# Kernel optimization log

Measured on AMD Instinct MI355X. Metric: run time of the kernel, lower is better.

Reference implementation:

```python
import math
import jax, jax.numpy as jnp
import numpy as np

B, S, HID, NH = 4, 1024, 768, 12
D = HID // NH
R_ACT = 0.5
R_ATTN = 0.5


def act_prune_mask(a, ratio):
    # per-sample kth-smallest magnitude threshold (torch.kthvalue on flatten(1))
    n = int(np.prod(a.shape[1:]))
    k = int(np.clip(n * ratio, 1, n))
    mag = jnp.abs(a)
    thr = jnp.sort(mag.reshape(a.shape[0], -1), axis=1)[:, k - 1]
    thr = thr.reshape((a.shape[0],) + (1,) * (a.ndim - 1))
    return mag >= thr


def setup_inputs() -> dict:
    key = jax.random.key(0)
    ks = jax.random.split(key, 5)
    inp = {
        "hidden_states": jax.random.normal(ks[0], (B, S, HID), dtype=jnp.float32),
        "Wq": jax.random.normal(ks[1], (HID, HID), dtype=jnp.float32) * 0.02,
        "bq": jnp.zeros((HID,), dtype=jnp.float32),
        "Wk": jax.random.normal(ks[2], (HID, HID), dtype=jnp.float32) * 0.02,
        "bk": jnp.zeros((HID,), dtype=jnp.float32),
        "Wv": jax.random.normal(ks[3], (HID, HID), dtype=jnp.float32) * 0.02,
        "bv": jnp.zeros((HID,), dtype=jnp.float32),
        "Wo": jax.random.normal(ks[4], (HID, HID), dtype=jnp.float32) * 0.02,
        "bo": jnp.zeros((HID,), dtype=jnp.float32),
    }
    return inp


def reference(hidden_states, Wq, bq, Wk, bk, Wv, bv, Wo, bo):
    b, s, hid = hidden_states.shape

    # prune mask on input activations (saved for backward in the original; forward math unchanged)
    mask_h = act_prune_mask(hidden_states, R_ACT)
    _hs_prune = jnp.where(mask_h, hidden_states, 0.0)

    q = jnp.matmul(hidden_states, Wq.T) + bq
    k = jnp.matmul(hidden_states, Wk.T) + bk
    v = jnp.matmul(hidden_states, Wv.T) + bv

    def split_heads(x):
        return x.reshape(b, s, NH, D).transpose(0, 2, 1, 3)  # [B,H,S,D]

    q4, k4, v4 = split_heads(q), split_heads(k), split_heads(v)

    mask_q = act_prune_mask(q4, R_ACT)
    mask_k = act_prune_mask(k4, R_ACT)
    _qp = jnp.where(mask_q, q4, 0.0)
    _kp = jnp.where(mask_k, k4, 0.0)

    scores = jnp.einsum("bhqd,bhkd->bhqk", q4, k4) / math.sqrt(D)
    probs = jax.nn.softmax(scores, axis=-1)

    mask_p = act_prune_mask(probs, R_ATTN)
    _pp = jnp.where(mask_p, probs, 0.0)
    mask_v = act_prune_mask(v4, R_ACT)
    _vp = jnp.where(mask_v, v4, 0.0)

    ctx = jnp.einsum("bhqk,bhkd->bhqd", probs, v4)
    ctx = ctx.transpose(0, 2, 1, 3).reshape(b, s, hid)

    mask_c = act_prune_mask(ctx, R_ACT)
    _cp = jnp.where(mask_c, ctx, 0.0)

    out = jnp.matmul(ctx, Wo.T) + bo  # proj_dropout rate = 0.0 (identity)
    return (out, probs)  # vis=True -> weights = attention_probs
```

## Files before the change

kernel.cpp:

```cpp
#include <hip/hip_runtime.h>
#include <hip/hip_bf16.h>

typedef __attribute__((ext_vector_type(4))) float f32x4;
typedef __attribute__((ext_vector_type(8))) short bf16x8;
typedef __attribute__((ext_vector_type(4))) int i32x4;

#define SEQ 1024
#define HIDV 768
#define NH 12
#define HD 64
#define QBLK 64

static __device__ __forceinline__ unsigned short f2b(float f) {
  unsigned u = __builtin_bit_cast(unsigned, f);
  u = (u + 0x7fffu + ((u >> 16) & 1u)) >> 16;
  return (unsigned short)u;
}

static __device__ __forceinline__ void gl16(const unsigned short* g, unsigned short* l) {
  __builtin_amdgcn_global_load_lds(
      (const __attribute__((address_space(1))) unsigned int*)g,
      (__attribute__((address_space(3))) unsigned int*)l, 16, 0, 0);
}

static __device__ __forceinline__ void bar_lgkm() {
  asm volatile("s_waitcnt lgkmcnt(0)" ::: "memory");
  __builtin_amdgcn_sched_barrier(0);
  __builtin_amdgcn_s_barrier();
  __builtin_amdgcn_sched_barrier(0);
}
static __device__ __forceinline__ void bar_only() {
  __builtin_amdgcn_sched_barrier(0);
  __builtin_amdgcn_s_barrier();
  __builtin_amdgcn_sched_barrier(0);
}

__global__ __launch_bounds__(256) void convert_all(
    const float* __restrict__ X, const float* __restrict__ Wq,
    const float* __restrict__ Wk, const float* __restrict__ Wv,
    const float* __restrict__ Wo, unsigned short* __restrict__ dst) {
  long i = (long)blockIdx.x * 256 + threadIdx.x;
  const long N4 = (3145728L + 4 * 589824L) / 4;
  if (i >= N4) return;
  long e = i * 4;
  const float* src; long off;
  if (e < 3145728L)      { src = X;  off = e; }
  else if (e < 3735552L) { src = Wq; off = e - 3145728L; }
  else if (e < 4325376L) { src = Wk; off = e - 3735552L; }
  else if (e < 4915200L) { src = Wv; off = e - 4325376L; }
  else                   { src = Wo; off = e - 4915200L; }
  const float4 v = *reinterpret_cast<const float4*>(src + off);
  ushort4 o;
  o.x = f2b(v.x); o.y = f2b(v.y); o.z = f2b(v.z); o.w = f2b(v.w);
  *reinterpret_cast<ushort4*>(dst + e) = o;
}

__global__ __launch_bounds__(256) void qkv_gemm(
    const unsigned short* __restrict__ Xb,
    const unsigned short* __restrict__ Wqb, const unsigned short* __restrict__ Wkb,
    const unsigned short* __restrict__ Wvb,
    const float* __restrict__ bq, const float* __restrict__ bk, const float* __restrict__ bv,
    unsigned short* __restrict__ Qh, unsigned short* __restrict__ Kh,
    unsigned short* __restrict__ VT) {
  __shared__ __align__(16) unsigned short la[128 * 32];
  __shared__ __align__(16) unsigned short lb[128 * 32];
  const int z = blockIdx.z;
  const unsigned short* Wb = (z == 0) ? Wqb : (z == 1) ? Wkb : Wvb;
  const float* bias = (z == 0) ? bq : (z == 1) ? bk : bv;
  const int m0 = blockIdx.x * 128, n0 = blockIdx.y * 128;
  const int tid = threadIdx.x;
  const int wave = tid >> 6, lane = tid & 63, g = lane >> 4, c = lane & 15;
  const int wr = (wave >> 1) * 64, wc = (wave & 1) * 64;

  const int sr = wave * 16 + (lane >> 2);
  const int scol = (lane & 3) * 8;
  const unsigned short* Ag = &Xb[(size_t)(m0 + sr) * HIDV + scol];
  const unsigned short* Bg = &Wb[(size_t)(n0 + sr) * HIDV + scol];
  unsigned short* lA0 = &la[(wave * 16) * 32];
  unsigned short* lA1 = &la[(64 + wave * 16) * 32];
  unsigned short* lB0 = &lb[(wave * 16) * 32];
  unsigned short* lB1 = &lb[(64 + wave * 16) * 32];

  f32x4 acc[4][4] = {};
  for (int kt = 0; kt < HIDV; kt += 32) {
    __syncthreads();
    gl16(Ag + kt, lA0);
    gl16(Ag + (size_t)64 * HIDV + kt, lA1);
    gl16(Bg + kt, lB0);
    gl16(Bg + (size_t)64 * HIDV + kt, lB1);
    __syncthreads();
    bf16x8 af[4], bfr[4];
#pragma unroll
    for (int m = 0; m < 4; m++)
      af[m] = *reinterpret_cast<bf16x8*>(&la[(wr + m * 16 + c) * 32 + g * 8]);
#pragma unroll
    for (int n = 0; n < 4; n++)
      bfr[n] = *reinterpret_cast<bf16x8*>(&lb[(wc + n * 16 + c) * 32 + g * 8]);
#pragma unroll
    for (int m = 0; m < 4; m++)
#pragma unroll
      for (int n = 0; n < 4; n++)
        acc[m][n] = __builtin_amdgcn_mfma_f32_16x16x32_bf16(af[m], bfr[n], acc[m][n], 0, 0, 0);
  }
  float bv4[4];
#pragma unroll
  for (int n = 0; n < 4; n++) bv4[n] = bias[n0 + wc + n * 16 + c];
  if (z < 2) {
    unsigned short* dst = (z == 0) ? Qh : Kh;
#pragma unroll
    for (int m = 0; m < 4; m++) {
      int rb_ = m0 + wr + m * 16 + g * 4;
#pragma unroll
      for (int n = 0; n < 4; n++) {
        int col = n0 + wc + n * 16 + c;
        int h = col >> 6, d = col & 63;
#pragma unroll
        for (int r = 0; r < 4; r++) {
          int row = rb_ + r;
          int b = row >> 10, s = row & 1023;
          dst[((size_t)(b * NH + h) * SEQ + s) * HD + d] = f2b(acc[m][n][r] + bv4[n]);
        }
      }
    }
  } else {
#pragma unroll
    for (int m = 0; m < 4; m++) {
      int rb_ = m0 + wr + m * 16 + g * 4;
      int b = rb_ >> 10, s = rb_ & 1023;
#pragma unroll
      for (int n = 0; n < 4; n++) {
        int col = n0 + wc + n * 16 + c;
        int h = col >> 6, d = col & 63;
        ushort4 o;
        o.x = f2b(acc[m][n][0] + bv4[n]);
        o.y = f2b(acc[m][n][1] + bv4[n]);
        o.z = f2b(acc[m][n][2] + bv4[n]);
        o.w = f2b(acc[m][n][3] + bv4[n]);
        *reinterpret_cast<ushort4*>(&VT[((size_t)(b * NH + h) * HD + d) * SEQ + s]) = o;
      }
    }
  }
}

#define EXPC 0.18033688f
__global__ __launch_bounds__(256) void attn_fused(
    const unsigned short* __restrict__ Qh, const unsigned short* __restrict__ Kh,
    const unsigned short* __restrict__ VT,
    float* __restrict__ probs, unsigned short* __restrict__ CTX) {
  __shared__ __align__(16) unsigned short ldsk[2][64 * 72];
  __shared__ __align__(16) unsigned short ldsv[2][64 * 72];
  __shared__ __align__(16) unsigned short lp[64 * 72];
  const int bh = blockIdx.y, rb = blockIdx.x * QBLK;
  const int b = bh / NH, h = bh - b * NH;
  const unsigned short* Qp = Qh + (size_t)bh * SEQ * HD;
  const unsigned short* Kp = Kh + (size_t)bh * SEQ * HD;
  const unsigned short* Vp = VT + (size_t)bh * HD * SEQ;
  float* P = probs + (size_t)bh * SEQ * SEQ;
  const int tid = threadIdx.x, wave = tid >> 6, lane = tid & 63, g = lane >> 4, c = lane & 15;
  const int wrow = wave * 16;
  const int str = tid >> 3;
  const int stc = (tid & 7) * 8;

  bf16x8 aq[2];
#pragma unroll
  for (int ks = 0; ks < 2; ks++)
    aq[ks] = *reinterpret_cast<const bf16x8*>(&Qp[(size_t)(rb + wrow + c) * HD + ks * 32 + g * 8]);

  i32x4 kr0, kr1, vr0, vr1;
  kr0 = *reinterpret_cast<const i32x4*>(&Kp[(size_t)str * HD + stc]);
  kr1 = *reinterpret_cast<const i32x4*>(&Kp[(size_t)(str + 32) * HD + stc]);
  *reinterpret_cast<i32x4*>(&ldsk[0][str * 72 + stc]) = kr0;
  *reinterpret_cast<i32x4*>(&ldsk[0][(str + 32) * 72 + stc]) = kr1;
  bar_lgkm();

  float lsum = 0.f;
  for (int ct = 0; ct < 16; ct++) {
    const int cur = ct & 1;
    if (ct < 15) {
      kr0 = *reinterpret_cast<const i32x4*>(&Kp[(size_t)((ct + 1) * 64 + str) * HD + stc]);
      kr1 = *reinterpret_cast<const i32x4*>(&Kp[(size_t)((ct + 1) * 64 + str + 32) * HD + stc]);
    }
    f32x4 sreg[4] = {};
#pragma unroll
    for (int ks = 0; ks < 2; ks++) {
      bf16x8 kf[4];
#pragma unroll
      for (int kb = 0; kb < 4; kb++)
        kf[kb] = *reinterpret_cast<bf16x8*>(&ldsk[cur][(kb * 16 + c) * 72 + ks * 32 + g * 8]);
#pragma unroll
      for (int kb = 0; kb < 4; kb++)
        sreg[kb] = __builtin_amdgcn_mfma_f32_16x16x32_bf16(kf[kb], aq[ks], sreg[kb], 0, 0, 0);
    }
#pragma unroll
    for (int kb = 0; kb < 4; kb++)
#pragma unroll
      for (int r = 0; r < 4; r++)
        lsum += __builtin_amdgcn_exp2f(sreg[kb][r] * EXPC);
    if (ct < 15) {
      *reinterpret_cast<i32x4*>(&ldsk[cur ^ 1][str * 72 + stc]) = kr0;
      *reinterpret_cast<i32x4*>(&ldsk[cur ^ 1][(str + 32) * 72 + stc]) = kr1;
      bar_lgkm();
    }
  }
  float s = lsum;
  s += __shfl_xor(s, 16);
  s += __shfl_xor(s, 32);
  const float linv = 1.f / s;

  kr0 = *reinterpret_cast<const i32x4*>(&Kp[(size_t)str * HD + stc]);
  kr1 = *reinterpret_cast<const i32x4*>(&Kp[(size_t)(str + 32) * HD + stc]);
  vr0 = *reinterpret_cast<const i32x4*>(&Vp[(size_t)str * SEQ + stc]);
  vr1 = *reinterpret_cast<const i32x4*>(&Vp[(size_t)(str + 32) * SEQ + stc]);
  *reinterpret_cast<i32x4*>(&ldsk[0][str * 72 + stc]) = kr0;
  *reinterpret_cast<i32x4*>(&ldsk[0][(str + 32) * 72 + stc]) = kr1;
  *reinterpret_cast<i32x4*>(&ldsv[0][str * 72 + stc]) = vr0;
  *reinterpret_cast<i32x4*>(&ldsv[0][(str + 32) * 72 + stc]) = vr1;
  bar_lgkm();

  f32x4 acc[4] = {};
  for (int ct = 0; ct < 16; ct++) {
    const int cur = ct & 1;
    if (ct < 15) {
      kr0 = *reinterpret_cast<const i32x4*>(&Kp[(size_t)((ct + 1) * 64 + str) * HD + stc]);
      kr1 = *reinterpret_cast<const i32x4*>(&Kp[(size_t)((ct + 1) * 64 + str + 32) * HD + stc]);
      vr0 = *reinterpret_cast<const i32x4*>(&Vp[(size_t)str * SEQ + (ct + 1) * 64 + stc]);
      vr1 = *reinterpret_cast<const i32x4*>(&Vp[(size_t)(str + 32) * SEQ + (ct + 1) * 64 + stc]);
    }
    f32x4 sreg[4] = {};
#pragma unroll
    for (int ks = 0; ks < 2; ks++) {
      bf16x8 kf[4];
#pragma unroll
      for (int kb = 0; kb < 4; kb++)
        kf[kb] = *reinterpret_cast<bf16x8*>(&ldsk[cur][(kb * 16 + c) * 72 + ks * 32 + g * 8]);
#pragma unroll
      for (int kb = 0; kb < 4; kb++)
        sreg[kb] = __builtin_amdgcn_mfma_f32_16x16x32_bf16(kf[kb], aq[ks], sreg[kb], 0, 0, 0);
    }
    {
      float* Prow = &P[(size_t)(rb + wrow + c) * SEQ + ct * 64];
#pragma unroll
      for (int kb = 0; kb < 4; kb++) {
        f32x4 p;
#pragma unroll
        for (int r = 0; r < 4; r++)
          p[r] = __builtin_amdgcn_exp2f(sreg[kb][r] * EXPC) * linv;
        *reinterpret_cast<f32x4*>(&Prow[kb * 16 + g * 4]) = p;
        uint2 pk;
        pk.x = (unsigned)f2b(p[0]) | ((unsigned)f2b(p[1]) << 16);
        pk.y = (unsigned)f2b(p[2]) | ((unsigned)f2b(p[3]) << 16);
        *reinterpret_cast<uint2*>(&lp[(wrow + c) * 72 + kb * 16 + g * 4]) = pk;
      }
    }
    if (ct < 15) {
      *reinterpret_cast<i32x4*>(&ldsk[cur ^ 1][str * 72 + stc]) = kr0;
      *reinterpret_cast<i32x4*>(&ldsk[cur ^ 1][(str + 32) * 72 + stc]) = kr1;
      *reinterpret_cast<i32x4*>(&ldsv[cur ^ 1][str * 72 + stc]) = vr0;
      *reinterpret_cast<i32x4*>(&ldsv[cur ^ 1][(str + 32) * 72 + stc]) = vr1;
    }
    bar_lgkm();
#pragma unroll
    for (int ks = 0; ks < 2; ks++) {
      bf16x8 pa, vf[4];
      pa = *reinterpret_cast<bf16x8*>(&lp[(wrow + c) * 72 + ks * 32 + g * 8]);
#pragma unroll
      for (int db = 0; db < 4; db++)
        vf[db] = *reinterpret_cast<bf16x8*>(&ldsv[cur][(db * 16 + c) * 72 + ks * 32 + g * 8]);
#pragma unroll
      for (int db = 0; db < 4; db++)
        acc[db] = __builtin_amdgcn_mfma_f32_16x16x32_bf16(pa, vf[db], acc[db], 0, 0, 0);
    }
    bar_only();
  }

#pragma unroll
  for (int db = 0; db < 4; db++)
#pragma unroll
    for (int r = 0; r < 4; r++)
      lp[(wrow + g * 4 + r) * 72 + db * 16 + c] = f2b(acc[db][r]);
  bar_lgkm();
  {
    const int q = tid >> 2, seg = (tid & 3) * 16;
    const unsigned short* src = &lp[q * 72 + seg];
    unsigned short* dst = &CTX[(size_t)(b * SEQ + rb + q) * HIDV + h * HD + seg];
    i32x4 t0 = *reinterpret_cast<const i32x4*>(&src[0]);
    i32x4 t1 = *reinterpret_cast<const i32x4*>(&src[8]);
    *reinterpret_cast<i32x4*>(&dst[0]) = t0;
    *reinterpret_cast<i32x4*>(&dst[8]) = t1;
  }
}

__global__ __launch_bounds__(256) void proj_gemm(
    const unsigned short* __restrict__ Ab, const unsigned short* __restrict__ Wb,
    const float* __restrict__ bias, float* __restrict__ out) {
  __shared__ __align__(16) unsigned short la[128 * 32];
  __shared__ __align__(16) unsigned short lb[128 * 32];
  const int m0 = blockIdx.x * 128, n0 = blockIdx.y * 128;
  const int tid = threadIdx.x;
  const int wave = tid >> 6, lane = tid & 63, g = lane >> 4, c = lane & 15;
  const int wr = (wave >> 1) * 64, wc = (wave & 1) * 64;
  const int sr = wave * 16 + (lane >> 2);
  const int scol = (lane & 3) * 8;
  const unsigned short* Ag = &Ab[(size_t)(m0 + sr) * HIDV + scol];
  const unsigned short* Bg = &Wb[(size_t)(n0 + sr) * HIDV + scol];
  unsigned short* lA0 = &la[(wave * 16) * 32];
  unsigned short* lA1 = &la[(64 + wave * 16) * 32];
  unsigned short* lB0 = &lb[(wave * 16) * 32];
  unsigned short* lB1 = &lb[(64 + wave * 16) * 32];

  f32x4 acc[4][4] = {};
  for (int kt = 0; kt < HIDV; kt += 32) {
    __syncthreads();
    gl16(Ag + kt, lA0);
    gl16(Ag + (size_t)64 * HIDV + kt, lA1);
    gl16(Bg + kt, lB0);
    gl16(Bg + (size_t)64 * HIDV + kt, lB1);
    __syncthreads();
    bf16x8 af[4], bfr[4];
#pragma unroll
    for (int m = 0; m < 4; m++)
      af[m] = *reinterpret_cast<bf16x8*>(&la[(wr + m * 16 + c) * 32 + g * 8]);
#pragma unroll
    for (int n = 0; n < 4; n++)
      bfr[n] = *reinterpret_cast<bf16x8*>(&lb[(wc + n * 16 + c) * 32 + g * 8]);
#pragma unroll
    for (int m = 0; m < 4; m++)
#pragma unroll
      for (int n = 0; n < 4; n++)
        acc[m][n] = __builtin_amdgcn_mfma_f32_16x16x32_bf16(af[m], bfr[n], acc[m][n], 0, 0, 0);
  }
  float bv4[4];
#pragma unroll
  for (int n = 0; n < 4; n++) bv4[n] = bias[n0 + wc + n * 16 + c];
#pragma unroll
  for (int m = 0; m < 4; m++) {
    int rb_ = m0 + wr + m * 16 + g * 4;
#pragma unroll
    for (int n = 0; n < 4; n++) {
      int col = n0 + wc + n * 16 + c;
#pragma unroll
      for (int r = 0; r < 4; r++)
        out[(size_t)(rb_ + r) * HIDV + col] = acc[m][n][r] + bv4[n];
    }
  }
}

extern "C" void kernel_launch(void* const* d_in, const int* in_sizes, int n_in,
                              void* d_out, int out_size, void* d_ws, size_t ws_size,
                              hipStream_t stream) {
  const float* X  = (const float*)d_in[0];
  const float* Wq = (const float*)d_in[1];
  const float* bq = (const float*)d_in[2];
  const float* Wk = (const float*)d_in[3];
  const float* bk = (const float*)d_in[4];
  const float* Wv = (const float*)d_in[5];
  const float* bv = (const float*)d_in[6];
  const float* Wo = (const float*)d_in[7];
  const float* bo = (const float*)d_in[8];
  float* out = (float*)d_out;
  float* probs = out + 3145728;

  unsigned short* Xb  = (unsigned short*)d_ws;
  unsigned short* Wqb = Xb + 3145728;
  unsigned short* Wkb = Wqb + 589824;
  unsigned short* Wvb = Wkb + 589824;
  unsigned short* Wob = Wvb + 589824;
  unsigned short* Qh  = Wob + 589824;
  unsigned short* Kh  = Qh + 3145728;
  unsigned short* VT  = Kh + 3145728;
  unsigned short* CTX = VT + 3145728;

  convert_all<<<5376, 256, 0, stream>>>(X, Wq, Wk, Wv, Wo, Xb);
  qkv_gemm<<<dim3(32, 6, 3), 256, 0, stream>>>(Xb, Wqb, Wkb, Wvb, bq, bk, bv, Qh, Kh, VT);
  attn_fused<<<dim3(16, 48), 256, 0, stream>>>(Qh, Kh, VT, probs, CTX);
  proj_gemm<<<dim3(32, 6), 256, 0, stream>>>(CTX, Wob, bo, out);
}
```

Before: 126.9 us.

## Double-buffer GEMM LDS tiles and read attention K/V directly from global

```diff
diff --git a/kernel.cpp b/kernel.cpp
--- a/kernel.cpp
+++ b/kernel.cpp
@@ -21,18 +21,6 @@
   __builtin_amdgcn_global_load_lds(
       (const __attribute__((address_space(1))) unsigned int*)g,
       (__attribute__((address_space(3))) unsigned int*)l, 16, 0, 0);
-}
-
-static __device__ __forceinline__ void bar_lgkm() {
-  asm volatile("s_waitcnt lgkmcnt(0)" ::: "memory");
-  __builtin_amdgcn_sched_barrier(0);
-  __builtin_amdgcn_s_barrier();
-  __builtin_amdgcn_sched_barrier(0);
-}
-static __device__ __forceinline__ void bar_only() {
-  __builtin_amdgcn_sched_barrier(0);
-  __builtin_amdgcn_s_barrier();
-  __builtin_amdgcn_sched_barrier(0);
 }
 
 __global__ __launch_bounds__(256) void convert_all(
@@ -62,8 +50,8 @@
     const float* __restrict__ bq, const float* __restrict__ bk, const float* __restrict__ bv,
     unsigned short* __restrict__ Qh, unsigned short* __restrict__ Kh,
     unsigned short* __restrict__ VT) {
-  __shared__ __align__(16) unsigned short la[128 * 32];
-  __shared__ __align__(16) unsigned short lb[128 * 32];
+  __shared__ __align__(16) unsigned short la[2][128 * 32];
+  __shared__ __align__(16) unsigned short lb[2][128 * 32];
   const int z = blockIdx.z;
   const unsigned short* Wb = (z == 0) ? Wqb : (z == 1) ? Wkb : Wvb;
   const float* bias = (z == 0) ? bq : (z == 1) ? bk : bv;
@@ -76,31 +64,36 @@
   const int scol = (lane & 3) * 8;
   const unsigned short* Ag = &Xb[(size_t)(m0 + sr) * HIDV + scol];
   const unsigned short* Bg = &Wb[(size_t)(n0 + sr) * HIDV + scol];
-  unsigned short* lA0 = &la[(wave * 16) * 32];
-  unsigned short* lA1 = &la[(64 + wave * 16) * 32];
-  unsigned short* lB0 = &lb[(wave * 16) * 32];
-  unsigned short* lB1 = &lb[(64 + wave * 16) * 32];
+
+  gl16(Ag, &la[0][(wave * 16) * 32]);
+  gl16(Ag + (size_t)64 * HIDV, &la[0][(64 + wave * 16) * 32]);
+  gl16(Bg, &lb[0][(wave * 16) * 32]);
+  gl16(Bg + (size_t)64 * HIDV, &lb[0][(64 + wave * 16) * 32]);
+  __syncthreads();
 
   f32x4 acc[4][4] = {};
-  for (int kt = 0; kt < HIDV; kt += 32) {
-    __syncthreads();
-    gl16(Ag + kt, lA0);
-    gl16(Ag + (size_t)64 * HIDV + kt, lA1);
-    gl16(Bg + kt, lB0);
-    gl16(Bg + (size_t)64 * HIDV + kt, lB1);
-    __syncthreads();
+  for (int t = 0; t < 24; t++) {
+    const int cur = t & 1;
+    if (t < 23) {
+      const int kt = (t + 1) * 32;
+      gl16(Ag + kt, &la[cur ^ 1][(wave * 16) * 32]);
+      gl16(Ag + (size_t)64 * HIDV + kt, &la[cur ^ 1][(64 + wave * 16) * 32]);
+      gl16(Bg + kt, &lb[cur ^ 1][(wave * 16) * 32]);
+      gl16(Bg + (size_t)64 * HIDV + kt, &lb[cur ^ 1][(64 + wave * 16) * 32]);
+    }
     bf16x8 af[4], bfr[4];
 #pragma unroll
     for (int m = 0; m < 4; m++)
-      af[m] = *reinterpret_cast<bf16x8*>(&la[(wr + m * 16 + c) * 32 + g * 8]);
+      af[m] = *reinterpret_cast<bf16x8*>(&la[cur][(wr + m * 16 + c) * 32 + g * 8]);
 #pragma unroll
     for (int n = 0; n < 4; n++)
-      bfr[n] = *reinterpret_cast<bf16x8*>(&lb[(wc + n * 16 + c) * 32 + g * 8]);
+      bfr[n] = *reinterpret_cast<bf16x8*>(&lb[cur][(wc + n * 16 + c) * 32 + g * 8]);
 #pragma unroll
     for (int m = 0; m < 4; m++)
 #pragma unroll
       for (int n = 0; n < 4; n++)
         acc[m][n] = __builtin_amdgcn_mfma_f32_16x16x32_bf16(af[m], bfr[n], acc[m][n], 0, 0, 0);
+    __syncthreads();
   }
   float bv4[4];
 #pragma unroll
@@ -147,9 +140,7 @@
     const unsigned short* __restrict__ Qh, const unsigned short* __restrict__ Kh,
     const unsigned short* __restrict__ VT,
     float* __restrict__ probs, unsigned short* __restrict__ CTX) {
-  __shared__ __align__(16) unsigned short ldsk[2][64 * 72];
-  __shared__ __align__(16) unsigned short ldsv[2][64 * 72];
-  __shared__ __align__(16) unsigned short lp[64 * 72];
+  __shared__ __align__(16) unsigned short lp[4][16 * 72];
   const int bh = blockIdx.y, rb = blockIdx.x * QBLK;
   const int b = bh / NH, h = bh - b * NH;
   const unsigned short* Qp = Qh + (size_t)bh * SEQ * HD;
@@ -157,36 +148,24 @@
   const unsigned short* Vp = VT + (size_t)bh * HD * SEQ;
   float* P = probs + (size_t)bh * SEQ * SEQ;
   const int tid = threadIdx.x, wave = tid >> 6, lane = tid & 63, g = lane >> 4, c = lane & 15;
-  const int wrow = wave * 16;
-  const int str = tid >> 3;
-  const int stc = (tid & 7) * 8;
+  const int qrow = rb + wave * 16 + c;
+  unsigned short* myp = &lp[wave][0];
 
   bf16x8 aq[2];
 #pragma unroll
   for (int ks = 0; ks < 2; ks++)
-    aq[ks] = *reinterpret_cast<const bf16x8*>(&Qp[(size_t)(rb + wrow + c) * HD + ks * 32 + g * 8]);
-
-  i32x4 kr0, kr1, vr0, vr1;
-  kr0 = *reinterpret_cast<const i32x4*>(&Kp[(size_t)str * HD + stc]);
-  kr1 = *reinterpret_cast<const i32x4*>(&Kp[(size_t)(str + 32) * HD + stc]);
-  *reinterpret_cast<i32x4*>(&ldsk[0][str * 72 + stc]) = kr0;
-  *reinterpret_cast<i32x4*>(&ldsk[0][(str + 32) * 72 + stc]) = kr1;
-  bar_lgkm();
+    aq[ks] = *reinterpret_cast<const bf16x8*>(&Qp[(size_t)qrow * HD + ks * 32 + g * 8]);
 
   float lsum = 0.f;
   for (int ct = 0; ct < 16; ct++) {
-    const int cur = ct & 1;
-    if (ct < 15) {
-      kr0 = *reinterpret_cast<const i32x4*>(&Kp[(size_t)((ct + 1) * 64 + str) * HD + stc]);
-      kr1 = *reinterpret_cast<const i32x4*>(&Kp[(size_t)((ct + 1) * 64 + str + 32) * HD + stc]);
-    }
     f32x4 sreg[4] = {};
 #pragma unroll
     for (int ks = 0; ks < 2; ks++) {
       bf16x8 kf[4];
 #pragma unroll
       for (int kb = 0; kb < 4; kb++)
-        kf[kb] = *reinterpret_cast<bf16x8*>(&ldsk[cur][(kb * 16 + c) * 72 + ks * 32 + g * 8]);
+        kf[kb] = *reinterpret_cast<const bf16x8*>(
+            &Kp[(size_t)(ct * 64 + kb * 16 + c) * HD + ks * 32 + g * 8]);
 #pragma unroll
       for (int kb = 0; kb < 4; kb++)
         sreg[kb] = __builtin_amdgcn_mfma_f32_16x16x32_bf16(kf[kb], aq[ks], sreg[kb], 0, 0, 0);
@@ -196,49 +175,28 @@
 #pragma unroll
       for (int r = 0; r < 4; r++)
         lsum += __builtin_amdgcn_exp2f(sreg[kb][r] * EXPC);
-    if (ct < 15) {
-      *reinterpret_cast<i32x4*>(&ldsk[cur ^ 1][str * 72 + stc]) = kr0;
-      *reinterpret_cast<i32x4*>(&ldsk[cur ^ 1][(str + 32) * 72 + stc]) = kr1;
-      bar_lgkm();
-    }
   }
   float s = lsum;
   s += __shfl_xor(s, 16);
   s += __shfl_xor(s, 32);
   const float linv = 1.f / s;
 
-  kr0 = *reinterpret_cast<const i32x4*>(&Kp[(size_t)str * HD + stc]);
-  kr1 = *reinterpret_cast<const i32x4*>(&Kp[(size_t)(str + 32) * HD + stc]);
-  vr0 = *reinterpret_cast<const i32x4*>(&Vp[(size_t)str * SEQ + stc]);
-  vr1 = *reinterpret_cast<const i32x4*>(&Vp[(size_t)(str + 32) * SEQ + stc]);
-  *reinterpret_cast<i32x4*>(&ldsk[0][str * 72 + stc]) = kr0;
-  *reinterpret_cast<i32x4*>(&ldsk[0][(str + 32) * 72 + stc]) = kr1;
-  *reinterpret_cast<i32x4*>(&ldsv[0][str * 72 + stc]) = vr0;
-  *reinterpret_cast<i32x4*>(&ldsv[0][(str + 32) * 72 + stc]) = vr1;
-  bar_lgkm();
-
   f32x4 acc[4] = {};
   for (int ct = 0; ct < 16; ct++) {
-    const int cur = ct & 1;
-    if (ct < 15) {
-      kr0 = *reinterpret_cast<const i32x4*>(&Kp[(size_t)((ct + 1) * 64 + str) * HD + stc]);
-      kr1 = *reinterpret_cast<const i32x4*>(&Kp[(size_t)((ct + 1) * 64 + str + 32) * HD + stc]);
-      vr0 = *reinterpret_cast<const i32x4*>(&Vp[(size_t)str * SEQ + (ct + 1) * 64 + stc]);
-      vr1 = *reinterpret_cast<const i32x4*>(&Vp[(size_t)(str + 32) * SEQ + (ct + 1) * 64 + stc]);
-    }
     f32x4 sreg[4] = {};
 #pragma unroll
     for (int ks = 0; ks < 2; ks++) {
       bf16x8 kf[4];
 #pragma unroll
       for (int kb = 0; kb < 4; kb++)
-        kf[kb] = *reinterpret_cast<bf16x8*>(&ldsk[cur][(kb * 16 + c) * 72 + ks * 32 + g * 8]);
+        kf[kb] = *reinterpret_cast<const bf16x8*>(
+            &Kp[(size_t)(ct * 64 + kb * 16 + c) * HD + ks * 32 + g * 8]);
 #pragma unroll
       for (int kb = 0; kb < 4; kb++)
         sreg[kb] = __builtin_amdgcn_mfma_f32_16x16x32_bf16(kf[kb], aq[ks], sreg[kb], 0, 0, 0);
     }
     {
-      float* Prow = &P[(size_t)(rb + wrow + c) * SEQ + ct * 64];
+      float* Prow = &P[(size_t)qrow * SEQ + ct * 64];
 #pragma unroll
       for (int kb = 0; kb < 4; kb++) {
         f32x4 p;
@@ -249,40 +207,32 @@
         uint2 pk;
         pk.x = (unsigned)f2b(p[0]) | ((unsigned)f2b(p[1]) << 16);
         pk.y = (unsigned)f2b(p[2]) | ((unsigned)f2b(p[3]) << 16);
-        *reinterpret_cast<uint2*>(&lp[(wrow + c) * 72 + kb * 16 + g * 4]) = pk;
+        *reinterpret_cast<uint2*>(&myp[c * 72 + kb * 16 + g * 4]) = pk;
       }
     }
-    if (ct < 15) {
-      *reinterpret_cast<i32x4*>(&ldsk[cur ^ 1][str * 72 + stc]) = kr0;
-      *reinterpret_cast<i32x4*>(&ldsk[cur ^ 1][(str + 32) * 72 + stc]) = kr1;
-      *reinterpret_cast<i32x4*>(&ldsv[cur ^ 1][str * 72 + stc]) = vr0;
-      *reinterpret_cast<i32x4*>(&ldsv[cur ^ 1][(str + 32) * 72 + stc]) = vr1;
-    }
-    bar_lgkm();
 #pragma unroll
     for (int ks = 0; ks < 2; ks++) {
       bf16x8 pa, vf[4];
-      pa = *reinterpret_cast<bf16x8*>(&lp[(wrow + c) * 72 + ks * 32 + g * 8]);
+      pa = *reinterpret_cast<bf16x8*>(&myp[c * 72 + ks * 32 + g * 8]);
 #pragma unroll
       for (int db = 0; db < 4; db++)
-        vf[db] = *reinterpret_cast<bf16x8*>(&ldsv[cur][(db * 16 + c) * 72 + ks * 32 + g * 8]);
+        vf[db] = *reinterpret_cast<const bf16x8*>(
+            &Vp[(size_t)(db * 16 + c) * SEQ + ct * 64 + ks * 32 + g * 8]);
 #pragma unroll
       for (int db = 0; db < 4; db++)
         acc[db] = __builtin_amdgcn_mfma_f32_16x16x32_bf16(pa, vf[db], acc[db], 0, 0, 0);
     }
-    bar_only();
   }
 
 #pragma unroll
   for (int db = 0; db < 4; db++)
 #pragma unroll
     for (int r = 0; r < 4; r++)
-      lp[(wrow + g * 4 + r) * 72 + db * 16 + c] = f2b(acc[db][r]);
-  bar_lgkm();
+      myp[(g * 4 + r) * 72 + db * 16 + c] = f2b(acc[db][r]);
   {
-    const int q = tid >> 2, seg = (tid & 3) * 16;
-    const unsigned short* src = &lp[q * 72 + seg];
-    unsigned short* dst = &CTX[(size_t)(b * SEQ + rb + q) * HIDV + h * HD + seg];
+    const int q = lane >> 2, seg = (lane & 3) * 16;
+    const unsigned short* src = &myp[q * 72 + seg];
+    unsigned short* dst = &CTX[(size_t)(b * SEQ + rb + wave * 16 + q) * HIDV + h * HD + seg];
     i32x4 t0 = *reinterpret_cast<const i32x4*>(&src[0]);
     i32x4 t1 = *reinterpret_cast<const i32x4*>(&src[8]);
     *reinterpret_cast<i32x4*>(&dst[0]) = t0;
@@ -293,8 +243,8 @@
 __global__ __launch_bounds__(256) void proj_gemm(
     const unsigned short* __restrict__ Ab, const unsigned short* __restrict__ Wb,
     const float* __restrict__ bias, float* __restrict__ out) {
-  __shared__ __align__(16) unsigned short la[128 * 32];
-  __shared__ __align__(16) unsigned short lb[128 * 32];
+  __shared__ __align__(16) unsigned short la[2][128 * 32];
+  __shared__ __align__(16) unsigned short lb[2][128 * 32];
   const int m0 = blockIdx.x * 128, n0 = blockIdx.y * 128;
   const int tid = threadIdx.x;
   const int wave = tid >> 6, lane = tid & 63, g = lane >> 4, c = lane & 15;
@@ -303,31 +253,36 @@
   const int scol = (lane & 3) * 8;
   const unsigned short* Ag = &Ab[(size_t)(m0 + sr) * HIDV + scol];
   const unsigned short* Bg = &Wb[(size_t)(n0 + sr) * HIDV + scol];
-  unsigned short* lA0 = &la[(wave * 16) * 32];
-  unsigned short* lA1 = &la[(64 + wave * 16) * 32];
-  unsigned short* lB0 = &lb[(wave * 16) * 32];
-  unsigned short* lB1 = &lb[(64 + wave * 16) * 32];
+
+  gl16(Ag, &la[0][(wave * 16) * 32]);
+  gl16(Ag + (size_t)64 * HIDV, &la[0][(64 + wave * 16) * 32]);
+  gl16(Bg, &lb[0][(wave * 16) * 32]);
+  gl16(Bg + (size_t)64 * HIDV, &lb[0][(64 + wave * 16) * 32]);
+  __syncthreads();
 
   f32x4 acc[4][4] = {};
-  for (int kt = 0; kt < HIDV; kt += 32) {
-    __syncthreads();
-    gl16(Ag + kt, lA0);
-    gl16(Ag + (size_t)64 * HIDV + kt, lA1);
-    gl16(Bg + kt, lB0);
-    gl16(Bg + (size_t)64 * HIDV + kt, lB1);
-    __syncthreads();
+  for (int t = 0; t < 24; t++) {
+    const int cur = t & 1;
+    if (t < 23) {
+      const int kt = (t + 1) * 32;
+      gl16(Ag + kt, &la[cur ^ 1][(wave * 16) * 32]);
+      gl16(Ag + (size_t)64 * HIDV + kt, &la[cur ^ 1][(64 + wave * 16) * 32]);
+      gl16(Bg + kt, &lb[cur ^ 1][(wave * 16) * 32]);
+      gl16(Bg + (size_t)64 * HIDV + kt, &lb[cur ^ 1][(64 + wave * 16) * 32]);
+    }
     bf16x8 af[4], bfr[4];
 #pragma unroll
     for (int m = 0; m < 4; m++)
-      af[m] = *reinterpret_cast<bf16x8*>(&la[(wr + m * 16 + c) * 32 + g * 8]);
+      af[m] = *reinterpret_cast<bf16x8*>(&la[cur][(wr + m * 16 + c) * 32 + g * 8]);
 #pragma unroll
     for (int n = 0; n < 4; n++)
-      bfr[n] = *reinterpret_cast<bf16x8*>(&lb[(wc + n * 16 + c) * 32 + g * 8]);
+      bfr[n] = *reinterpret_cast<bf16x8*>(&lb[cur][(wc + n * 16 + c) * 32 + g * 8]);
 #pragma unroll
     for (int m = 0; m < 4; m++)
 #pragma unroll
       for (int n = 0; n < 4; n++)
         acc[m][n] = __builtin_amdgcn_mfma_f32_16x16x32_bf16(af[m], bfr[n], acc[m][n], 0, 0, 0);
+    __syncthreads();
   }
   float bv4[4];
 #pragma unroll
```

After: 200.7 us. 58.2% more time.

## Double-buffer LDS in QKV/projection GEMMs and swizzle attention block order

Applied to the files above, without the earlier changes.

```diff
diff --git a/kernel.cpp b/kernel.cpp
--- a/kernel.cpp
+++ b/kernel.cpp
@@ -62,8 +62,8 @@
     const float* __restrict__ bq, const float* __restrict__ bk, const float* __restrict__ bv,
     unsigned short* __restrict__ Qh, unsigned short* __restrict__ Kh,
     unsigned short* __restrict__ VT) {
-  __shared__ __align__(16) unsigned short la[128 * 32];
-  __shared__ __align__(16) unsigned short lb[128 * 32];
+  __shared__ __align__(16) unsigned short la[2][128 * 32];
+  __shared__ __align__(16) unsigned short lb[2][128 * 32];
   const int z = blockIdx.z;
   const unsigned short* Wb = (z == 0) ? Wqb : (z == 1) ? Wkb : Wvb;
   const float* bias = (z == 0) ? bq : (z == 1) ? bk : bv;
@@ -76,31 +76,36 @@
   const int scol = (lane & 3) * 8;
   const unsigned short* Ag = &Xb[(size_t)(m0 + sr) * HIDV + scol];
   const unsigned short* Bg = &Wb[(size_t)(n0 + sr) * HIDV + scol];
-  unsigned short* lA0 = &la[(wave * 16) * 32];
-  unsigned short* lA1 = &la[(64 + wave * 16) * 32];
-  unsigned short* lB0 = &lb[(wave * 16) * 32];
-  unsigned short* lB1 = &lb[(64 + wave * 16) * 32];
+
+  gl16(Ag, &la[0][(wave * 16) * 32]);
+  gl16(Ag + (size_t)64 * HIDV, &la[0][(64 + wave * 16) * 32]);
+  gl16(Bg, &lb[0][(wave * 16) * 32]);
+  gl16(Bg + (size_t)64 * HIDV, &lb[0][(64 + wave * 16) * 32]);
+  __syncthreads();
 
   f32x4 acc[4][4] = {};
-  for (int kt = 0; kt < HIDV; kt += 32) {
-    __syncthreads();
-    gl16(Ag + kt, lA0);
-    gl16(Ag + (size_t)64 * HIDV + kt, lA1);
-    gl16(Bg + kt, lB0);
-    gl16(Bg + (size_t)64 * HIDV + kt, lB1);
-    __syncthreads();
+  for (int t = 0; t < 24; t++) {
+    const int cur = t & 1;
+    if (t < 23) {
+      const int kt = (t + 1) * 32;
+      gl16(Ag + kt, &la[cur ^ 1][(wave * 16) * 32]);
+      gl16(Ag + (size_t)64 * HIDV + kt, &la[cur ^ 1][(64 + wave * 16) * 32]);
+      gl16(Bg + kt, &lb[cur ^ 1][(wave * 16) * 32]);
+      gl16(Bg + (size_t)64 * HIDV + kt, &lb[cur ^ 1][(64 + wave * 16) * 32]);
+    }
     bf16x8 af[4], bfr[4];
 #pragma unroll
     for (int m = 0; m < 4; m++)
-      af[m] = *reinterpret_cast<bf16x8*>(&la[(wr + m * 16 + c) * 32 + g * 8]);
+      af[m] = *reinterpret_cast<bf16x8*>(&la[cur][(wr + m * 16 + c) * 32 + g * 8]);
 #pragma unroll
     for (int n = 0; n < 4; n++)
-      bfr[n] = *reinterpret_cast<bf16x8*>(&lb[(wc + n * 16 + c) * 32 + g * 8]);
+      bfr[n] = *reinterpret_cast<bf16x8*>(&lb[cur][(wc + n * 16 + c) * 32 + g * 8]);
 #pragma unroll
     for (int m = 0; m < 4; m++)
 #pragma unroll
       for (int n = 0; n < 4; n++)
         acc[m][n] = __builtin_amdgcn_mfma_f32_16x16x32_bf16(af[m], bfr[n], acc[m][n], 0, 0, 0);
+    __syncthreads();
   }
   float bv4[4];
 #pragma unroll
@@ -150,7 +155,9 @@
   __shared__ __align__(16) unsigned short ldsk[2][64 * 72];
   __shared__ __align__(16) unsigned short ldsv[2][64 * 72];
   __shared__ __align__(16) unsigned short lp[64 * 72];
-  const int bh = blockIdx.y, rb = blockIdx.x * QBLK;
+  const int lin = blockIdx.x;
+  const int swz = (lin & 7) * 96 + (lin >> 3);
+  const int bh = swz >> 4, rb = (swz & 15) * QBLK;
   const int b = bh / NH, h = bh - b * NH;
   const unsigned short* Qp = Qh + (size_t)bh * SEQ * HD;
   const unsigned short* Kp = Kh + (size_t)bh * SEQ * HD;
@@ -293,8 +300,8 @@
 __global__ __launch_bounds__(256) void proj_gemm(
     const unsigned short* __restrict__ Ab, const unsigned short* __restrict__ Wb,
     const float* __restrict__ bias, float* __restrict__ out) {
-  __shared__ __align__(16) unsigned short la[128 * 32];
-  __shared__ __align__(16) unsigned short lb[128 * 32];
+  __shared__ __align__(16) unsigned short la[2][128 * 32];
+  __shared__ __align__(16) unsigned short lb[2][128 * 32];
   const int m0 = blockIdx.x * 128, n0 = blockIdx.y * 128;
   const int tid = threadIdx.x;
   const int wave = tid >> 6, lane = tid & 63, g = lane >> 4, c = lane & 15;
@@ -303,31 +310,36 @@
   const int scol = (lane & 3) * 8;
   const unsigned short* Ag = &Ab[(size_t)(m0 + sr) * HIDV + scol];
   const unsigned short* Bg = &Wb[(size_t)(n0 + sr) * HIDV + scol];
-  unsigned short* lA0 = &la[(wave * 16) * 32];
-  unsigned short* lA1 = &la[(64 + wave * 16) * 32];
-  unsigned short* lB0 = &lb[(wave * 16) * 32];
-  unsigned short* lB1 = &lb[(64 + wave * 16) * 32];
+
+  gl16(Ag, &la[0][(wave * 16) * 32]);
+  gl16(Ag + (size_t)64 * HIDV, &la[0][(64 + wave * 16) * 32]);
+  gl16(Bg, &lb[0][(wave * 16) * 32]);
+  gl16(Bg + (size_t)64 * HIDV, &lb[0][(64 + wave * 16) * 32]);
+  __syncthreads();
 
   f32x4 acc[4][4] = {};
-  for (int kt = 0; kt < HIDV; kt += 32) {
-    __syncthreads();
-    gl16(Ag + kt, lA0);
-    gl16(Ag + (size_t)64 * HIDV + kt, lA1);
-    gl16(Bg + kt, lB0);
-    gl16(Bg + (size_t)64 * HIDV + kt, lB1);
-    __syncthreads();
+  for (int t = 0; t < 24; t++) {
+    const int cur = t & 1;
+    if (t < 23) {
+      const int kt = (t + 1) * 32;
+      gl16(Ag + kt, &la[cur ^ 1][(wave * 16) * 32]);
+      gl16(Ag + (size_t)64 * HIDV + kt, &la[cur ^ 1][(64 + wave * 16) * 32]);
+      gl16(Bg + kt, &lb[cur ^ 1][(wave * 16) * 32]);
+      gl16(Bg + (size_t)64 * HIDV + kt, &lb[cur ^ 1][(64 + wave * 16) * 32]);
+    }
     bf16x8 af[4], bfr[4];
 #pragma unroll
     for (int m = 0; m < 4; m++)
-      af[m] = *reinterpret_cast<bf16x8*>(&la[(wr + m * 16 + c) * 32 + g * 8]);
+      af[m] = *reinterpret_cast<bf16x8*>(&la[cur][(wr + m * 16 + c) * 32 + g * 8]);
 #pragma unroll
     for (int n = 0; n < 4; n++)
-      bfr[n] = *reinterpret_cast<bf16x8*>(&lb[(wc + n * 16 + c) * 32 + g * 8]);
+      bfr[n] = *reinterpret_cast<bf16x8*>(&lb[cur][(wc + n * 16 + c) * 32 + g * 8]);
 #pragma unroll
     for (int m = 0; m < 4; m++)
 #pragma unroll
       for (int n = 0; n < 4; n++)
         acc[m][n] = __builtin_amdgcn_mfma_f32_16x16x32_bf16(af[m], bfr[n], acc[m][n], 0, 0, 0);
+    __syncthreads();
   }
   float bv4[4];
 #pragma unroll
@@ -372,6 +384,6 @@
 
   convert_all<<<5376, 256, 0, stream>>>(X, Wq, Wk, Wv, Wo, Xb);
   qkv_gemm<<<dim3(32, 6, 3), 256, 0, stream>>>(Xb, Wqb, Wkb, Wvb, bq, bk, bv, Qh, Kh, VT);
-  attn_fused<<<dim3(16, 48), 256, 0, stream>>>(Qh, Kh, VT, probs, CTX);
+  attn_fused<<<dim3(768), 256, 0, stream>>>(Qh, Kh, VT, probs, CTX);
   proj_gemm<<<dim3(32, 6), 256, 0, stream>>>(CTX, Wob, bo, out);
 }
```

Result: faster. 113.4 us (-10.6%).
